# Performance work log

Hardware: AMD Instinct MI355X
Metric: run time of the kernel (lower is better)

## Reference

```python
import jax, jax.numpy as jnp
import numpy as np

N_EMBD = 1024
HEAD_SIZE = 64

def setup_inputs() -> dict:
    key = jax.random.key(0)
    kx, kk, kq, kv = jax.random.split(key, 4)
    B, T = 8, 2048
    x = jax.random.normal(kx, (B, T, N_EMBD), dtype=jnp.float32)
    s = 1.0 / np.sqrt(N_EMBD)  # torch Linear default init scale (kaiming-uniform-ish)
    Wk = jax.random.uniform(kk, (N_EMBD, HEAD_SIZE), jnp.float32, -s, s)
    Wq = jax.random.uniform(kq, (N_EMBD, HEAD_SIZE), jnp.float32, -s, s)
    Wv = jax.random.uniform(kv, (N_EMBD, HEAD_SIZE), jnp.float32, -s, s)
    return {"x": x, "Wk": Wk, "Wq": Wq, "Wv": Wv}

def reference(x, Wk, Wq, Wv):
    # x: (B,T,C); projections to (B,T,H)
    k = jnp.einsum('btc,ch->bth', x, Wk)
    q = jnp.einsum('btc,ch->bth', x, Wq)
    v = jnp.einsum('btc,ch->bth', x, Wv)
    T = x.shape[1]
    scale = k.shape[-1] ** -0.5
    wei = jnp.einsum('bth,bsh->bts', q, k) * scale  # (B,T,T)
    causal = jnp.tril(jnp.ones((T, T), dtype=bool))
    wei = jnp.where(causal, wei, -jnp.inf)
    wei = jax.nn.softmax(wei, axis=-1)
    out = jnp.einsum('bts,bsh->bth', wei, v)  # (B,T,H)
    return out
```

## Files before the change

kernel.cpp:

```cpp
#include <hip/hip_runtime.h>
#include <math.h>

namespace {
constexpr int BATCH = 8;
constexpr int TSEQ  = 2048;
constexpr int CDIM  = 1024;
constexpr int HDIM  = 64;
constexpr int MROWS = BATCH * TSEQ;
constexpr int NTILE = 128;
constexpr int NSLC  = 8;
constexpr float QSCALE = 0.125f * 1.4426950408889634f;
}

typedef __attribute__((ext_vector_type(4))) float  f32x4;
typedef __attribute__((ext_vector_type(8))) short  s16x8;
typedef __attribute__((ext_vector_type(4))) unsigned short u16x4;

__device__ __forceinline__ unsigned short f2bf(float f) {
    union { float f; unsigned u; } c{f};
    unsigned r = c.u + 0x7FFFu + ((c.u >> 16) & 1u);
    return (unsigned short)(r >> 16);
}
__device__ __forceinline__ float bf2f(unsigned short h) {
    union { unsigned u; float f; } c;
    c.u = (unsigned)h << 16;
    return c.f;
}

__device__ __forceinline__ void st_sys_b16(unsigned short* p, unsigned v) {
    asm volatile("global_store_short %0, %1, off sc0 sc1"
                 :: "v"((unsigned long long)(uintptr_t)p), "v"(v) : "memory");
}
__device__ __forceinline__ void st_sys_b32(float* p, float v) {
    asm volatile("global_store_dword %0, %1, off sc0 sc1"
                 :: "v"((unsigned long long)(uintptr_t)p), "v"(v) : "memory");
}

__global__ __launch_bounds__(256)
void wswz_kernel(const float* __restrict__ Wk, const float* __restrict__ Wq,
                 const float* __restrict__ Wv, unsigned short* __restrict__ swz,
                 unsigned* __restrict__ cnt)
{
    if (blockIdx.x == 0) cnt[threadIdx.x] = 0u;

    const int idx  = blockIdx.x * 256 + threadIdx.x;
    const int j    = idx & 7;
    const int lane = (idx >> 3) & 63;
    const int rest = idx >> 9;
    const int tn   = rest % 12;
    const int ksg  = rest / 12;
    const int kk   = ksg * 32 + (lane >> 4) * 8 + j;
    const int n    = tn * 16 + (lane & 15);
    float val;
    if (n < 64)       val = Wq[kk * HDIM + n] * QSCALE;
    else if (n < 128) val = Wk[kk * HDIM + (n - 64)];
    else              val = Wv[kk * HDIM + (n - 128)];
    swz[idx] = f2bf(val);
}

__global__ __launch_bounds__(256, 4)
void proj_kernel(const float* __restrict__ x, const unsigned short* __restrict__ swz,
                 unsigned short* __restrict__ q, unsigned short* __restrict__ k,
                 unsigned short* __restrict__ vt)
{
    __shared__ unsigned short xl[16][1032];

    const int tid  = threadIdx.x;
    const int lane = tid & 63, wave = tid >> 6;
    const int quad = lane >> 4, l15 = lane & 15;
    const int cq   = wave;
    const int m0   = blockIdx.x * 16;

    {
        const float* xb = x + (size_t)m0 * CDIM;
        float4 t[16];
        #pragma unroll
        for (int i = 0; i < 16; ++i)
            t[i] = *(const float4*)(xb + i * 1024 + tid * 4);
        #pragma unroll
        for (int i = 0; i < 16; ++i) {
            const int o = i * 1024 + tid * 4;
            u16x4 p;
            p[0] = f2bf(t[i].x); p[1] = f2bf(t[i].y);
            p[2] = f2bf(t[i].z); p[3] = f2bf(t[i].w);
            *(u16x4*)&xl[o >> 10][o & 1023] = p;
        }
    }
    __syncthreads();

    f32x4 acc[3] = {};
    const unsigned short* bp = swz + ((size_t)(cq * 3) * 64 + lane) * 8;
    s16x8 b0 = *(const s16x8*)(bp);
    s16x8 b1 = *(const s16x8*)(bp + 512);
    s16x8 b2 = *(const s16x8*)(bp + 1024);
    bp += 6144;

    #pragma unroll
    for (int ks = 0; ks < 32; ++ks) {
        s16x8 nb0, nb1, nb2;
        if (ks < 31) {
            nb0 = *(const s16x8*)(bp);
            nb1 = *(const s16x8*)(bp + 512);
            nb2 = *(const s16x8*)(bp + 1024);
            bp += 6144;
        }
        const s16x8 af = *(const s16x8*)&xl[l15][ks * 32 + quad * 8];
        acc[0] = __builtin_amdgcn_mfma_f32_16x16x32_bf16(af, b0, acc[0], 0, 0, 0);
        acc[1] = __builtin_amdgcn_mfma_f32_16x16x32_bf16(af, b1, acc[1], 0, 0, 0);
        acc[2] = __builtin_amdgcn_mfma_f32_16x16x32_bf16(af, b2, acc[2], 0, 0, 0);
        if (ks < 31) { b0 = nb0; b1 = nb1; b2 = nb2; }
    }

    const int rowg = m0 + quad * 4;
    #pragma unroll
    for (int t = 0; t < 3; ++t) {
        const int n = cq * 48 + t * 16 + l15;
        if (n < 64) {
            #pragma unroll
            for (int r = 0; r < 4; ++r)
                q[(size_t)(rowg + r) * HDIM + n] = f2bf(acc[t][r]);
        } else if (n < 128) {
            #pragma unroll
            for (int r = 0; r < 4; ++r)
                k[(size_t)(rowg + r) * HDIM + (n - 64)] = f2bf(acc[t][r]);
        } else {
            const int h  = n - 128;
            const int bb = rowg >> 11, tl = rowg & 2047;
            u16x4 pv;
            #pragma unroll
            for (int r = 0; r < 4; ++r) pv[r] = f2bf(acc[t][r]);
            *(u16x4*)(vt + ((size_t)bb * HDIM + h) * TSEQ + tl) = pv;
        }
    }
}

__device__ __forceinline__ void combine_tile(
    const unsigned short* __restrict__ Opart, const float* __restrict__ lpart,
    float* __restrict__ out, int b, int t, int valid, int tid)
{
    float a[4][4] = {{0.f}};
    float lv[4] = {0.f, 0.f, 0.f, 0.f};
    size_t lbase[4]; int rr[4], c4v[4];
    #pragma unroll
    for (int i = 0; i < 4; ++i) {
        const int item = i * 256 + tid;
        rr[i]  = item >> 4;
        c4v[i] = (item & 15) << 2;
        const int ti16 = t * 4 + (rr[i] >> 4);
        lbase[i] = ((size_t)b * NTILE + ti16) * NSLC * 16 + (rr[i] & 15);
    }
    for (int s = 0; s < valid; ++s) {
        unsigned long long o0, o1, o2, o3;
        float f0, f1, f2, f3;
        const unsigned long long A0 = (unsigned long long)(uintptr_t)(Opart + (lbase[0] + (size_t)s * 16) * HDIM + c4v[0]);
        const unsigned long long A1 = (unsigned long long)(uintptr_t)(Opart + (lbase[1] + (size_t)s * 16) * HDIM + c4v[1]);
        const unsigned long long A2 = (unsigned long long)(uintptr_t)(Opart + (lbase[2] + (size_t)s * 16) * HDIM + c4v[2]);
        const unsigned long long A3 = (unsigned long long)(uintptr_t)(Opart + (lbase[3] + (size_t)s * 16) * HDIM + c4v[3]);
        const unsigned long long L0 = (unsigned long long)(uintptr_t)(lpart + lbase[0] + (size_t)s * 16);
        const unsigned long long L1 = (unsigned long long)(uintptr_t)(lpart + lbase[1] + (size_t)s * 16);
        const unsigned long long L2 = (unsigned long long)(uintptr_t)(lpart + lbase[2] + (size_t)s * 16);
        const unsigned long long L3 = (unsigned long long)(uintptr_t)(lpart + lbase[3] + (size_t)s * 16);
        asm volatile(
            "global_load_dwordx2 %0, %8, off sc0 sc1\n\t"
            "global_load_dwordx2 %1, %9, off sc0 sc1\n\t"
            "global_load_dwordx2 %2, %10, off sc0 sc1\n\t"
            "global_load_dwordx2 %3, %11, off sc0 sc1\n\t"
            "global_load_dword %4, %12, off sc0 sc1\n\t"
            "global_load_dword %5, %13, off sc0 sc1\n\t"
            "global_load_dword %6, %14, off sc0 sc1\n\t"
            "global_load_dword %7, %15, off sc0 sc1\n\t"
            "s_waitcnt vmcnt(0)"
            : "=&v"(o0), "=&v"(o1), "=&v"(o2), "=&v"(o3),
              "=&v"(f0), "=&v"(f1), "=&v"(f2), "=&v"(f3)
            : "v"(A0), "v"(A1), "v"(A2), "v"(A3),
              "v"(L0), "v"(L1), "v"(L2), "v"(L3)
            : "memory");
        #pragma unroll
        for (int j = 0; j < 4; ++j) {
            a[0][j] += bf2f((unsigned short)(o0 >> (16 * j)));
            a[1][j] += bf2f((unsigned short)(o1 >> (16 * j)));
            a[2][j] += bf2f((unsigned short)(o2 >> (16 * j)));
            a[3][j] += bf2f((unsigned short)(o3 >> (16 * j)));
        }
        lv[0] += f0; lv[1] += f1; lv[2] += f2; lv[3] += f3;
    }
    #pragma unroll
    for (int i = 0; i < 4; ++i) {
        const float inv = 1.f / lv[i];
        float4 o = {a[i][0] * inv, a[i][1] * inv, a[i][2] * inv, a[i][3] * inv};
        const int row = b * TSEQ + t * 64 + rr[i];
        *(float4*)(out + (size_t)row * HDIM + c4v[i]) = o;
    }
}

__global__ __launch_bounds__(256, 4)
void attn_kernel(const unsigned short* __restrict__ q, const unsigned short* __restrict__ k,
                 const unsigned short* __restrict__ vt,
                 unsigned short* __restrict__ Opart, float* __restrict__ lpart,
                 unsigned* __restrict__ cnt, float* __restrict__ out)
{
    __shared__ unsigned short Kb[4096];
    __shared__ unsigned short Vb[4096];
    __shared__ unsigned short Pl[4][16][72];
    __shared__ int sflag;

    const int tid  = threadIdx.x;
    const int lane = tid & 63, wave = tid >> 6;
    const int quad = lane >> 4, l15 = lane & 15;
    const int b    = blockIdx.y;
    const int p    = blockIdx.x >> 3;
    const int s    = blockIdx.x & 7;

    const unsigned short* qb  = q  + (size_t)b * TSEQ * HDIM;
    const unsigned short* kb  = k  + (size_t)b * TSEQ * HDIM;
    const unsigned short* vtb = vt + (size_t)b * HDIM * TSEQ;

    const int rs = tid >> 3, cgs = tid & 7;
    const int d0 = (((cgs >> 2) * 4 + (rs >> 4)) * 64 + (cgs & 3) * 16 + (rs & 15)) * 8;
    const int rs2 = rs + 32;
    const int d1 = (((cgs >> 2) * 4 + (rs2 >> 4)) * 64 + (cgs & 3) * 16 + (rs2 & 15)) * 8;

    for (int tsel = 0; tsel < 2; ++tsel) {
        const int t   = (tsel == 0) ? p : 31 - p;
        const int m0w = t * 64 + wave * 16;
        const int nt  = t + 1;

        if (s < nt) {
            const s16x8 aq0 = *(const s16x8*)(qb + (size_t)(m0w + l15) * HDIM + quad * 8);
            const s16x8 aq1 = *(const s16x8*)(qb + (size_t)(m0w + l15) * HDIM + 32 + quad * 8);

            f32x4 O[4] = {};
            float l_lane[4] = {0.f, 0.f, 0.f, 0.f};

            {
                const int n0 = s * 64;
                const s16x8 ka = *(const s16x8*)(kb + (size_t)(n0 + rs) * HDIM + cgs * 8);
                const s16x8 kc = *(const s16x8*)(kb + (size_t)(n0 + rs2) * HDIM + cgs * 8);
                const s16x8 va = *(const s16x8*)(vtb + (size_t)rs * TSEQ + n0 + cgs * 8);
                const s16x8 vc = *(const s16x8*)(vtb + (size_t)rs2 * TSEQ + n0 + cgs * 8);
                *(s16x8*)&Kb[d0] = ka; *(s16x8*)&Kb[d1] = kc;
                *(s16x8*)&Vb[d0] = va; *(s16x8*)&Vb[d1] = vc;
            }
            __syncthreads();

            for (int c = s; c < nt; c += 8) {
                const bool pref = (c + 8) < nt;
                s16x8 ka, kc, va, vc;
                if (pref) {
                    const int n0n = (c + 8) * 64;
                    ka = *(const s16x8*)(kb + (size_t)(n0n + rs) * HDIM + cgs * 8);
                    kc = *(const s16x8*)(kb + (size_t)(n0n + rs2) * HDIM + cgs * 8);
                    va = *(const s16x8*)(vtb + (size_t)rs * TSEQ + n0n + cgs * 8);
                    vc = *(const s16x8*)(vtb + (size_t)rs2 * TSEQ + n0n + cgs * 8);
                }

                f32x4 S[4] = {};
                #pragma unroll
                for (int st = 0; st < 4; ++st) {
                    const s16x8 k0 = *(const s16x8*)&Kb[(st * 64 + lane) * 8];
                    const s16x8 k1 = *(const s16x8*)&Kb[((4 + st) * 64 + lane) * 8];
                    S[st] = __builtin_amdgcn_mfma_f32_16x16x32_bf16(aq0, k0, S[st], 0, 0, 0);
                    S[st] = __builtin_amdgcn_mfma_f32_16x16x32_bf16(aq1, k1, S[st], 0, 0, 0);
                }
                __syncthreads();
                if (pref) { *(s16x8*)&Kb[d0] = ka; *(s16x8*)&Kb[d1] = kc; }

                const int n0 = c * 64;
                if (c == t) {
                    const int rowbase = m0w + quad * 4;
                    #pragma unroll
                    for (int st = 0; st < 4; ++st) {
                        const int col = n0 + st * 16 + l15;
                        #pragma unroll
                        for (int r = 0; r < 4; ++r) {
                            const float pv = (col > rowbase + r) ? 0.f : exp2f(S[st][r]);
                            S[st][r] = pv;
                            l_lane[r] += pv;
                        }
                    }
                } else {
                    #pragma unroll
                    for (int st = 0; st < 4; ++st)
                        #pragma unroll
                        for (int r = 0; r < 4; ++r) {
                            const float pv = exp2f(S[st][r]);
                            S[st][r] = pv;
                            l_lane[r] += pv;
                        }
                }

                #pragma unroll
                for (int st = 0; st < 4; ++st)
                    #pragma unroll
                    for (int r = 0; r < 4; ++r)
                        Pl[wave][quad * 4 + r][st * 16 + l15] = f2bf(S[st][r]);
                const s16x8 pa0 = *(const s16x8*)&Pl[wave][l15][quad * 8];
                const s16x8 pa1 = *(const s16x8*)&Pl[wave][l15][32 + quad * 8];

                #pragma unroll
                for (int hst = 0; hst < 4; ++hst) {
                    const s16x8 v0 = *(const s16x8*)&Vb[(hst * 64 + lane) * 8];
                    const s16x8 v1 = *(const s16x8*)&Vb[((4 + hst) * 64 + lane) * 8];
                    O[hst] = __builtin_amdgcn_mfma_f32_16x16x32_bf16(pa0, v0, O[hst], 0, 0, 0);
                    O[hst] = __builtin_amdgcn_mfma_f32_16x16x32_bf16(pa1, v1, O[hst], 0, 0, 0);
                }
                __syncthreads();
                if (pref) { *(s16x8*)&Vb[d0] = va; *(s16x8*)&Vb[d1] = vc; }
            }

            #pragma unroll
            for (int off = 1; off < 16; off <<= 1)
                #pragma unroll
                for (int r = 0; r < 4; ++r)
                    l_lane[r] += __shfl_xor(l_lane[r], off);

            const int ti16 = t * 4 + wave;
            const size_t pi = ((size_t)b * NTILE + ti16) * NSLC + s;
            #pragma unroll
            for (int hst = 0; hst < 4; ++hst)
                #pragma unroll
                for (int r = 0; r < 4; ++r)
                    st_sys_b16(Opart + (pi * 16 + quad * 4 + r) * HDIM + hst * 16 + l15,
                               (unsigned)f2bf(O[hst][r]));
            if (l15 == 0) {
                #pragma unroll
                for (int r = 0; r < 4; ++r)
                    st_sys_b32(lpart + pi * 16 + quad * 4 + r, l_lane[r]);
            }
            asm volatile("s_waitcnt vmcnt(0)" ::: "memory");
            __syncthreads();

            const int valid = (nt < NSLC) ? nt : NSLC;
            if (tid == 0) {
                const unsigned old = __hip_atomic_fetch_add(
                    &cnt[b * 32 + t], 1u, __ATOMIC_RELAXED,
                    __HIP_MEMORY_SCOPE_AGENT);
                sflag = (old == (unsigned)(valid - 1));
            }
            __syncthreads();
            if (sflag)
                combine_tile(Opart, lpart, out, b, t, valid, tid);
        }
    }
}

extern "C" void kernel_launch(void* const* d_in, const int* in_sizes, int n_in,
                              void* d_out, int out_size, void* d_ws, size_t ws_size,
                              hipStream_t stream) {
    const float* x  = (const float*)d_in[0];
    const float* Wk = (const float*)d_in[1];
    const float* Wq = (const float*)d_in[2];
    const float* Wv = (const float*)d_in[3];
    float* out = (float*)d_out;

    unsigned short* swz = (unsigned short*)d_ws;
    unsigned short* qw  = swz + 196608;
    unsigned short* kw  = qw + (size_t)MROWS * HDIM;
    unsigned short* vtw = kw + (size_t)MROWS * HDIM;
    unsigned short* Opart = vtw + (size_t)MROWS * HDIM;
    float* lpart = (float*)(Opart + (size_t)BATCH * NTILE * NSLC * 16 * HDIM);
    unsigned* cnt = (unsigned*)(lpart + (size_t)BATCH * NTILE * NSLC * 16);

    wswz_kernel<<<dim3(768), 256, 0, stream>>>(Wk, Wq, Wv, swz, cnt);
    proj_kernel<<<dim3(MROWS / 16), 256, 0, stream>>>(x, swz, qw, kw, vtw);
    attn_kernel<<<dim3(16 * NSLC, BATCH), 256, 0, stream>>>(qw, kw, vtw,
                                                            Opart, lpart, cnt, out);
}
```

Baseline: 137.7 us.

## Process 32 rows per projection block to reuse weight fragments, XOR-swizzle LDS

The projection kernel now handles 32 rows of x per block instead of 16, so each weight fragment fetched from global memory feeds two MFMAs and the weight traffic per output row is halved. The LDS tile drops its padding and uses an XOR swizzle on columns to avoid bank conflicts. In exchange each block holds twice the accumulators and registers, the grid shrinks to 512 blocks, and the launch bound falls to 2 blocks per SIMD, which lowers occupancy.

```diff
diff --git a/kernel.cpp b/kernel.cpp
--- a/kernel.cpp
+++ b/kernel.cpp
@@ -58,43 +58,46 @@
     swz[idx] = f2bf(val);
 }
 
-__global__ __launch_bounds__(256, 4)
+__global__ __launch_bounds__(256, 2)
 void proj_kernel(const float* __restrict__ x, const unsigned short* __restrict__ swz,
                  unsigned short* __restrict__ q, unsigned short* __restrict__ k,
                  unsigned short* __restrict__ vt)
 {
-    __shared__ unsigned short xl[16][1032];
+    __shared__ unsigned short xl[32][1024];
 
     const int tid  = threadIdx.x;
     const int lane = tid & 63, wave = tid >> 6;
     const int quad = lane >> 4, l15 = lane & 15;
     const int cq   = wave;
-    const int m0   = blockIdx.x * 16;
-
-    {
-        const float* xb = x + (size_t)m0 * CDIM;
+    const int m0   = blockIdx.x * 32;
+
+    #pragma unroll
+    for (int pass = 0; pass < 2; ++pass) {
+        const float* xb = x + (size_t)(m0 + pass * 16) * CDIM;
         float4 t[16];
         #pragma unroll
         for (int i = 0; i < 16; ++i)
             t[i] = *(const float4*)(xb + i * 1024 + tid * 4);
         #pragma unroll
         for (int i = 0; i < 16; ++i) {
-            const int o = i * 1024 + tid * 4;
+            const int row = pass * 16 + i;
+            const int col = (tid * 4) ^ ((row & 7) << 3);
             u16x4 p;
             p[0] = f2bf(t[i].x); p[1] = f2bf(t[i].y);
             p[2] = f2bf(t[i].z); p[3] = f2bf(t[i].w);
-            *(u16x4*)&xl[o >> 10][o & 1023] = p;
+            *(u16x4*)&xl[row][col] = p;
         }
     }
     __syncthreads();
 
-    f32x4 acc[3] = {};
+    f32x4 acc[2][3] = {};
     const unsigned short* bp = swz + ((size_t)(cq * 3) * 64 + lane) * 8;
     s16x8 b0 = *(const s16x8*)(bp);
     s16x8 b1 = *(const s16x8*)(bp + 512);
     s16x8 b2 = *(const s16x8*)(bp + 1024);
     bp += 6144;
 
+    const int swzl = (l15 & 7) << 3;
     #pragma unroll
     for (int ks = 0; ks < 32; ++ks) {
         s16x8 nb0, nb1, nb2;
@@ -104,32 +107,40 @@
             nb2 = *(const s16x8*)(bp + 1024);
             bp += 6144;
         }
-        const s16x8 af = *(const s16x8*)&xl[l15][ks * 32 + quad * 8];
-        acc[0] = __builtin_amdgcn_mfma_f32_16x16x32_bf16(af, b0, acc[0], 0, 0, 0);
-        acc[1] = __builtin_amdgcn_mfma_f32_16x16x32_bf16(af, b1, acc[1], 0, 0, 0);
-        acc[2] = __builtin_amdgcn_mfma_f32_16x16x32_bf16(af, b2, acc[2], 0, 0, 0);
+        const int c = (ks * 32 + quad * 8) ^ swzl;
+        const s16x8 a0 = *(const s16x8*)&xl[l15][c];
+        const s16x8 a1 = *(const s16x8*)&xl[16 + l15][c];
+        acc[0][0] = __builtin_amdgcn_mfma_f32_16x16x32_bf16(a0, b0, acc[0][0], 0, 0, 0);
+        acc[1][0] = __builtin_amdgcn_mfma_f32_16x16x32_bf16(a1, b0, acc[1][0], 0, 0, 0);
+        acc[0][1] = __builtin_amdgcn_mfma_f32_16x16x32_bf16(a0, b1, acc[0][1], 0, 0, 0);
+        acc[1][1] = __builtin_amdgcn_mfma_f32_16x16x32_bf16(a1, b1, acc[1][1], 0, 0, 0);
+        acc[0][2] = __builtin_amdgcn_mfma_f32_16x16x32_bf16(a0, b2, acc[0][2], 0, 0, 0);
+        acc[1][2] = __builtin_amdgcn_mfma_f32_16x16x32_bf16(a1, b2, acc[1][2], 0, 0, 0);
         if (ks < 31) { b0 = nb0; b1 = nb1; b2 = nb2; }
     }
 
-    const int rowg = m0 + quad * 4;
-    #pragma unroll
-    for (int t = 0; t < 3; ++t) {
-        const int n = cq * 48 + t * 16 + l15;
-        if (n < 64) {
-            #pragma unroll
-            for (int r = 0; r < 4; ++r)
-                q[(size_t)(rowg + r) * HDIM + n] = f2bf(acc[t][r]);
-        } else if (n < 128) {
-            #pragma unroll
-            for (int r = 0; r < 4; ++r)
-                k[(size_t)(rowg + r) * HDIM + (n - 64)] = f2bf(acc[t][r]);
-        } else {
-            const int h  = n - 128;
-            const int bb = rowg >> 11, tl = rowg & 2047;
-            u16x4 pv;
-            #pragma unroll
-            for (int r = 0; r < 4; ++r) pv[r] = f2bf(acc[t][r]);
-            *(u16x4*)(vt + ((size_t)bb * HDIM + h) * TSEQ + tl) = pv;
+    #pragma unroll
+    for (int g = 0; g < 2; ++g) {
+        const int rowg = m0 + g * 16 + quad * 4;
+        #pragma unroll
+        for (int t = 0; t < 3; ++t) {
+            const int n = cq * 48 + t * 16 + l15;
+            if (n < 64) {
+                #pragma unroll
+                for (int r = 0; r < 4; ++r)
+                    q[(size_t)(rowg + r) * HDIM + n] = f2bf(acc[g][t][r]);
+            } else if (n < 128) {
+                #pragma unroll
+                for (int r = 0; r < 4; ++r)
+                    k[(size_t)(rowg + r) * HDIM + (n - 64)] = f2bf(acc[g][t][r]);
+            } else {
+                const int h  = n - 128;
+                const int bb = rowg >> 11, tl = rowg & 2047;
+                u16x4 pv;
+                #pragma unroll
+                for (int r = 0; r < 4; ++r) pv[r] = f2bf(acc[g][t][r]);
+                *(u16x4*)(vt + ((size_t)bb * HDIM + h) * TSEQ + tl) = pv;
+            }
         }
     }
 }
@@ -362,7 +373,7 @@
     unsigned* cnt = (unsigned*)(lpart + (size_t)BATCH * NTILE * NSLC * 16);
 
     wswz_kernel<<<dim3(768), 256, 0, stream>>>(Wk, Wq, Wv, swz, cnt);
-    proj_kernel<<<dim3(MROWS / 16), 256, 0, stream>>>(x, swz, qw, kw, vtw);
+    proj_kernel<<<dim3(MROWS / 32), 256, 0, stream>>>(x, swz, qw, kw, vtw);
     attn_kernel<<<dim3(16 * NSLC, BATCH), 256, 0, stream>>>(qw, kw, vtw,
                                                             Opart, lpart, cnt, out);
 }
```

Measured after the change: 137.6 us. About the same (-0.0%).
